# Optimization experiments

Measured on AMD Instinct MI355X. Metric: run time of the kernel, lower is better.

Reference implementation:

```python
import jax, jax.numpy as jnp
import numpy as np

N_NODES = 50000
N_EDGES = 800000
NDIM_IN = 128
EDIM_IN = 128
NDIM_OUT = 128
EDIM_OUT = 128


def setup_inputs() -> dict:
    key = jax.random.key(0)
    ks = jax.random.split(key, 8)
    nfeats = jax.random.normal(ks[0], (N_NODES, NDIM_IN), dtype=jnp.float32)
    efeats = jax.random.normal(ks[1], (N_EDGES, EDIM_IN), dtype=jnp.float32)
    u = jax.random.randint(ks[2], (N_EDGES,), 0, N_NODES, dtype=jnp.int32)
    v = jax.random.randint(ks[3], (N_EDGES,), 0, N_NODES, dtype=jnp.int32)
    # torch.nn.Linear params: weight [out, in], bias [out]
    d_apply_in = 2 * NDIM_IN + EDIM_IN  # concat(nfeats, h_neigh)
    lim1 = 1.0 / np.sqrt(d_apply_in)
    W_apply_w = jax.random.uniform(ks[4], (NDIM_OUT, d_apply_in), jnp.float32, -lim1, lim1)
    W_apply_b = jax.random.uniform(ks[5], (NDIM_OUT,), jnp.float32, -lim1, lim1)
    lim2 = 1.0 / np.sqrt(2 * NDIM_OUT)
    W_edge_w = jax.random.uniform(ks[6], (EDIM_OUT, 2 * NDIM_OUT), jnp.float32, -lim2, lim2)
    W_edge_b = jax.random.uniform(ks[7], (EDIM_OUT,), jnp.float32, -lim2, lim2)
    return {"nfeats": nfeats, "efeats": efeats, "u": u, "v": v,
            "W_apply_w": W_apply_w, "W_apply_b": W_apply_b,
            "W_edge_w": W_edge_w, "W_edge_b": W_edge_b}


def reference(nfeats, efeats, u, v, W_apply_w, W_apply_b, W_edge_w, W_edge_b):
    n_nodes = nfeats.shape[0]
    # message per edge: concat(src node h, edge h)  -> [E, ndim_in+edim_in]
    msg = jnp.concatenate([nfeats[u], efeats], axis=1)
    # mean reduction over incoming edges at dst node v (0 for isolated nodes, like DGL)
    sums = jax.ops.segment_sum(msg, v, num_segments=n_nodes)
    counts = jax.ops.segment_sum(jnp.ones((msg.shape[0],), msg.dtype), v, num_segments=n_nodes)
    h_neigh = jnp.where(counts[:, None] > 0, sums / jnp.maximum(counts, 1.0)[:, None], 0.0)
    # node update
    h_nodes_new = jnp.concatenate([nfeats, h_neigh], axis=1) @ W_apply_w.T + W_apply_b
    h_nodes_new = jax.nn.relu(h_nodes_new)
    # edge update
    edge_input = jnp.concatenate([h_nodes_new[u], h_nodes_new[v]], axis=1)
    h_edges_new = jax.nn.relu(edge_input @ W_edge_w.T + W_edge_b)
    return h_nodes_new, h_edges_new
```

## Files before the change

kernel.cpp:

```cpp
#include <hip/hip_runtime.h>
#include <hip/hip_bf16.h>

#define N_NODES_C 50000
#define N_EDGES_C 800000
#define NBLK_NODES 196
#define EDGE_HEAD_ROWS 50048

typedef __attribute__((ext_vector_type(8))) short bf16x8;
typedef __attribute__((ext_vector_type(4))) float f32x4;

__device__ __forceinline__ unsigned short f2bf(float f) {
    unsigned int x = __float_as_uint(f);
    unsigned int r = x + 0x7fffu + ((x >> 16) & 1u);
    return (unsigned short)(r >> 16);
}
__device__ __forceinline__ float bf2f(unsigned short s) {
    return __uint_as_float(((unsigned int)s) << 16);
}

__global__ __launch_bounds__(256) void setup_k(
    const float* __restrict__ Wa, const float* __restrict__ We,
    unsigned short* __restrict__ wa, unsigned short* __restrict__ we,
    int* __restrict__ cnt)
{
    int b = blockIdx.x, t = threadIdx.x;
    if (b < 196) {
        int i = b * 256 + t;
        if (i < N_NODES_C) cnt[i] = 0;
    } else if (b < 388) {
        int i = (b - 196) * 256 + t;
        wa[i] = f2bf(Wa[i]);
    } else {
        int i = (b - 388) * 256 + t;
        we[i] = f2bf(We[i]);
    }
}

__global__ __launch_bounds__(256) void count_k(const int* __restrict__ v, int* __restrict__ cnt)
{
    int e = blockIdx.x * 256 + threadIdx.x;
    atomicAdd(&cnt[v[e]], 1);
}

__global__ __launch_bounds__(256) void scan_partial_k(
    const int* __restrict__ cnt, int* __restrict__ bsum)
{
    __shared__ int ws[4];
    int b = blockIdx.x, t = threadIdx.x, lane = t & 63, wid = t >> 6;
    int i = b * 256 + t;
    int x = (i < N_NODES_C) ? cnt[i] : 0;
    int s = x;
#pragma unroll
    for (int d = 1; d < 64; d <<= 1) {
        int tv = __shfl_up(s, d, 64);
        if (lane >= d) s += tv;
    }
    if (lane == 63) ws[wid] = s;
    __syncthreads();
    if (t == 0) bsum[b] = ws[0] + ws[1] + ws[2] + ws[3];
}

__global__ __launch_bounds__(256) void scan_block_k(
    const int* __restrict__ bsum, int* __restrict__ boff, int* __restrict__ rowst)
{
    __shared__ int ws[4];
    int t = threadIdx.x, lane = t & 63, wid = t >> 6;
    int x = (t < NBLK_NODES) ? bsum[t] : 0;
    int s = x;
#pragma unroll
    for (int d = 1; d < 64; d <<= 1) {
        int tv = __shfl_up(s, d, 64);
        if (lane >= d) s += tv;
    }
    if (lane == 63) ws[wid] = s;
    __syncthreads();
    if (t == 0) {
        int a = 0;
#pragma unroll
        for (int w = 0; w < 4; ++w) { int tmp = ws[w]; ws[w] = a; a += tmp; }
    }
    __syncthreads();
    int excl = ws[wid] + s - x;
    if (t < NBLK_NODES) boff[t] = excl;
    if (t == 255) rowst[N_NODES_C] = excl;
}

__global__ __launch_bounds__(256) void scan_scatter_k(
    const int* __restrict__ cnt, const int* __restrict__ boff,
    int* __restrict__ rowst, int* __restrict__ cursor)
{
    __shared__ int ws[4];
    int b = blockIdx.x, t = threadIdx.x, lane = t & 63, wid = t >> 6;
    int i = b * 256 + t;
    int x = (i < N_NODES_C) ? cnt[i] : 0;
    int s = x;
#pragma unroll
    for (int d = 1; d < 64; d <<= 1) {
        int tv = __shfl_up(s, d, 64);
        if (lane >= d) s += tv;
    }
    if (lane == 63) ws[wid] = s;
    __syncthreads();
    if (t == 0) {
        int a = 0;
#pragma unroll
        for (int w = 0; w < 4; ++w) { int tmp = ws[w]; ws[w] = a; a += tmp; }
    }
    __syncthreads();
    int excl = boff[b] + ws[wid] + s - x;
    if (i < N_NODES_C) { rowst[i] = excl; cursor[i] = excl; }
}

__global__ __launch_bounds__(256) void fill_k(const int* __restrict__ v,
                                              const int* __restrict__ u,
                                              int* __restrict__ cursor,
                                              int2* __restrict__ pairs)
{
    int e = blockIdx.x * 256 + threadIdx.x;
    int pos = atomicAdd(&cursor[v[e]], 1);
    pairs[pos] = make_int2(e, u[e]);
}

__global__ __launch_bounds__(256) void aggregate_k(
    const int2* __restrict__ pairs, const int* __restrict__ rowst,
    const float* __restrict__ nfeats, const float* __restrict__ efeats,
    unsigned short* __restrict__ hnb)
{
    int wv   = blockIdx.x * 4 + (threadIdx.x >> 6);
    int lane = threadIdx.x & 63;
    if (wv >= N_NODES_C) return;
    int s = rowst[wv], e_end = rowst[wv + 1];
    int deg = e_end - s;

    if (deg == 0) {
        *reinterpret_cast<ushort4*>(hnb + (size_t)wv * 256 + lane * 4) =
            make_ushort4(0, 0, 0, 0);
        return;
    }

    float4 a0 = make_float4(0.f, 0.f, 0.f, 0.f);
    float4 a1 = a0, a2 = a0, a3 = a0;
    for (int base = s; base < e_end; base += 8) {
        int2 p[8];
#pragma unroll
        for (int t = 0; t < 8; ++t) {
            int idx = base + t;
            p[t] = pairs[idx < e_end ? idx : e_end - 1];
        }
        float4 val[8];
#pragma unroll
        for (int t = 0; t < 8; ++t) {
            const float* src = (lane < 32)
                ? (nfeats + (size_t)p[t].y * 128 + lane * 4)
                : (efeats + (size_t)p[t].x * 128 + (lane - 32) * 4);
            val[t] = *reinterpret_cast<const float4*>(src);
        }
#pragma unroll
        for (int t = 0; t < 8; ++t) {
            if (base + t < e_end) {
                float4* a = (t & 2) ? ((t & 1) ? &a3 : &a2)
                                    : ((t & 1) ? &a1 : &a0);
                a->x += val[t].x; a->y += val[t].y;
                a->z += val[t].z; a->w += val[t].w;
            }
        }
    }
    a0.x += a1.x + a2.x + a3.x;
    a0.y += a1.y + a2.y + a3.y;
    a0.z += a1.z + a2.z + a3.z;
    a0.w += a1.w + a2.w + a3.w;
    float r = 1.f / (float)deg;
    ushort4 o;
    o.x = f2bf(a0.x * r); o.y = f2bf(a0.y * r);
    o.z = f2bf(a0.z * r); o.w = f2bf(a0.w * r);
    *reinterpret_cast<ushort4*>(hnb + (size_t)wv * 256 + lane * 4) = o;
}

__device__ __forceinline__ void stage_half_row(
    const float* __restrict__ src, char* __restrict__ lds, int row, int halfg)
{
#pragma unroll
    for (int g = 0; g < 4; ++g) {
        float4 f0 = reinterpret_cast<const float4*>(src)[g * 2 + 0];
        float4 f1 = reinterpret_cast<const float4*>(src)[g * 2 + 1];
        union { unsigned short s[8]; uint4 q; } pk;
        pk.s[0] = f2bf(f0.x); pk.s[1] = f2bf(f0.y);
        pk.s[2] = f2bf(f0.z); pk.s[3] = f2bf(f0.w);
        pk.s[4] = f2bf(f1.x); pk.s[5] = f2bf(f1.y);
        pk.s[6] = f2bf(f1.z); pk.s[7] = f2bf(f1.w);
        int byteoff = ((halfg * 4 + g) * 16) ^ ((row & 7) << 4);
        *reinterpret_cast<uint4*>(lds + row * 128 + byteoff) = pk.q;
    }
}

__device__ __forceinline__ void stage_half_row_cp(
    const unsigned short* __restrict__ src, char* __restrict__ lds, int row, int halfg)
{
#pragma unroll
    for (int g = 0; g < 4; ++g) {
        uint4 q = reinterpret_cast<const uint4*>(src)[g];
        int byteoff = ((halfg * 4 + g) * 16) ^ ((row & 7) << 4);
        *reinterpret_cast<uint4*>(lds + row * 128 + byteoff) = q;
    }
}

__device__ __forceinline__ void mfma_slab(
    const char* __restrict__ Xs, const char* __restrict__ Ws,
    int wm, int wn, int lane, f32x4 (&acc)[4][4])
{
#pragma unroll
    for (int c = 0; c < 2; ++c) {
        int kb = c * 64 + (lane >> 4) * 16;
        bf16x8 a[4], b[4];
#pragma unroll
        for (int i = 0; i < 4; ++i) {
            int row = wm * 64 + i * 16 + (lane & 15);
            a[i] = *reinterpret_cast<const bf16x8*>(
                Xs + row * 128 + (kb ^ ((row & 7) << 4)));
        }
#pragma unroll
        for (int j = 0; j < 4; ++j) {
            int row = wn * 64 + j * 16 + (lane & 15);
            b[j] = *reinterpret_cast<const bf16x8*>(
                Ws + row * 128 + (kb ^ ((row & 7) << 4)));
        }
#pragma unroll
        for (int i = 0; i < 4; ++i)
#pragma unroll
            for (int j = 0; j < 4; ++j)
                acc[i][j] = __builtin_amdgcn_mfma_f32_16x16x32_bf16(
                    a[i], b[j], acc[i][j], 0, 0, 0);
    }
}

__device__ __forceinline__ void epilogue_store(
    const f32x4 (&acc)[4][4], const float* __restrict__ bias,
    float* __restrict__ out, int row_base, int row_limit, int wm, int wn, int lane)
{
    int col0 = wn * 64 + (lane & 15);
    int row0 = row_base + wm * 64 + (lane >> 4) * 4;
#pragma unroll
    for (int j = 0; j < 4; ++j) {
        float bj = bias[col0 + j * 16];
#pragma unroll
        for (int i = 0; i < 4; ++i) {
#pragma unroll
            for (int r = 0; r < 4; ++r) {
                int row = row0 + i * 16 + r;
                if (row < row_limit) {
                    float val = fmaxf(acc[i][j][r] + bj, 0.f);
                    out[(size_t)row * 128 + col0 + j * 16] = val;
                }
            }
        }
    }
}

__global__ __launch_bounds__(256) void node_k(
    const float* __restrict__ nfeats, const unsigned short* __restrict__ hnb,
    const unsigned short* __restrict__ wa, const unsigned short* __restrict__ we,
    const float* __restrict__ bias, float* __restrict__ out,
    unsigned short* __restrict__ P)
{
    __shared__ uint4 XsBuf[1024];
    __shared__ uint4 WsBuf[1024];
    char* Xs = (char*)XsBuf;
    char* Ws = (char*)WsBuf;

    int tid = threadIdx.x;
    int n0  = blockIdx.x * 128;
    int wave = tid >> 6, lane = tid & 63;
    int wm = wave >> 1, wn = wave & 1;
    int srow = tid >> 1, shalf = tid & 1;

    int nrow = n0 + srow;
    if (nrow >= N_NODES_C) nrow = N_NODES_C - 1;

    f32x4 acc[4][4];
#pragma unroll
    for (int i = 0; i < 4; ++i)
#pragma unroll
        for (int j = 0; j < 4; ++j) acc[i][j] = (f32x4)0.f;

#pragma unroll
    for (int k0 = 0; k0 < 384; k0 += 64) {
        if (k0 < 128)
            stage_half_row(nfeats + (size_t)nrow * 128 + k0 + shalf * 32,
                           Xs, srow, shalf);
        else
            stage_half_row_cp(hnb + (size_t)nrow * 256 + (k0 - 128) + shalf * 32,
                              Xs, srow, shalf);
        stage_half_row_cp(wa + (size_t)srow * 384 + k0 + shalf * 32,
                          Ws, srow, shalf);
        __syncthreads();
        mfma_slab(Xs, Ws, wm, wn, lane, acc);
        __syncthreads();
    }

    epilogue_store(acc, bias, out, n0, N_NODES_C, wm, wn, lane);
    __syncthreads();

    int col0 = wn * 64 + (lane & 15);
    int row0 = n0 + wm * 64 + (lane >> 4) * 4;
#pragma unroll
    for (int cb = 0; cb < 2; ++cb) {
        f32x4 accP[4][4];
#pragma unroll
        for (int i = 0; i < 4; ++i)
#pragma unroll
            for (int j = 0; j < 4; ++j) accP[i][j] = (f32x4)0.f;

#pragma unroll
        for (int s2 = 0; s2 < 2; ++s2) {
            int k0 = s2 * 64;
            stage_half_row(out + (size_t)nrow * 128 + k0 + shalf * 32,
                           Xs, srow, shalf);
            stage_half_row_cp(we + (size_t)srow * 256 + cb * 128 + k0 + shalf * 32,
                              Ws, srow, shalf);
            __syncthreads();
            mfma_slab(Xs, Ws, wm, wn, lane, accP);
            __syncthreads();
        }

#pragma unroll
        for (int j = 0; j < 4; ++j) {
#pragma unroll
            for (int i = 0; i < 4; ++i) {
#pragma unroll
                for (int r = 0; r < 4; ++r) {
                    int row = row0 + i * 16 + r;
                    if (row < N_NODES_C)
                        P[(size_t)row * 256 + cb * 128 + col0 + j * 16] =
                            f2bf(accP[i][j][r]);
                }
            }
        }
    }
}

__global__ __launch_bounds__(256) void edge_add_k(
    const unsigned short* __restrict__ P, const int* __restrict__ u,
    const int* __restrict__ v, const float* __restrict__ bias,
    float* __restrict__ out, int e_base)
{
    int c = blockIdx.x * 256 + threadIdx.x;
    int e = e_base + (c >> 5);
    int q = c & 31;
    int uu = u[e], vv = v[e];
    ushort4 pa = *reinterpret_cast<const ushort4*>(P + (size_t)uu * 256 + q * 4);
    ushort4 pb = *reinterpret_cast<const ushort4*>(P + (size_t)vv * 256 + 128 + q * 4);
    float4 b4 = *reinterpret_cast<const float4*>(bias + q * 4);
    float4 o;
    o.x = fmaxf(bf2f(pa.x) + bf2f(pb.x) + b4.x, 0.f);
    o.y = fmaxf(bf2f(pa.y) + bf2f(pb.y) + b4.y, 0.f);
    o.z = fmaxf(bf2f(pa.z) + bf2f(pb.z) + b4.z, 0.f);
    o.w = fmaxf(bf2f(pa.w) + bf2f(pb.w) + b4.w, 0.f);
    *reinterpret_cast<float4*>(out + (size_t)e * 128 + q * 4) = o;
}

__global__ __launch_bounds__(256) void edge_head_k(
    const float* __restrict__ h, const int* __restrict__ u,
    const int* __restrict__ v, const float* __restrict__ W,
    const float* __restrict__ bias, float* __restrict__ out)
{
    __shared__ uint4 XsBuf[1024];
    __shared__ uint4 WsBuf[1024];
    __shared__ int us[128], vs[128];
    char* Xs = (char*)XsBuf;
    char* Ws = (char*)WsBuf;

    int tid = threadIdx.x;
    int e0  = blockIdx.x * 128;
    if (tid < 128) us[tid]       = u[e0 + tid];
    else           vs[tid - 128] = v[e0 + tid - 128];
    __syncthreads();

    int wave = tid >> 6, lane = tid & 63;
    int wm = wave >> 1, wn = wave & 1;
    int srow = tid >> 1, shalf = tid & 1;

    f32x4 acc[4][4];
#pragma unroll
    for (int i = 0; i < 4; ++i)
#pragma unroll
        for (int j = 0; j < 4; ++j) acc[i][j] = (f32x4)0.f;

#pragma unroll
    for (int k0 = 0; k0 < 256; k0 += 64) {
        int node = (k0 < 128) ? us[srow] : vs[srow];
        stage_half_row(h + (size_t)node * 128 + (k0 & 127) + shalf * 32,
                       Xs, srow, shalf);
        stage_half_row(W + (size_t)srow * 256 + k0 + shalf * 32,
                       Ws, srow, shalf);
        __syncthreads();
        mfma_slab(Xs, Ws, wm, wn, lane, acc);
        __syncthreads();
    }

    epilogue_store(acc, bias, out, e0, N_EDGES_C, wm, wn, lane);
}

extern "C" void kernel_launch(void* const* d_in, const int* in_sizes, int n_in,
                              void* d_out, int out_size, void* d_ws, size_t ws_size,
                              hipStream_t stream)
{
    const float* nfeats    = (const float*)d_in[0];
    const float* efeats    = (const float*)d_in[1];
    const int*   u         = (const int*)d_in[2];
    const int*   v         = (const int*)d_in[3];
    const float* W_apply_w = (const float*)d_in[4];
    const float* W_apply_b = (const float*)d_in[5];
    const float* W_edge_w  = (const float*)d_in[6];
    const float* W_edge_b  = (const float*)d_in[7];

    float* out      = (float*)d_out;
    float* h_nodes  = out;
    float* edge_out = out + (size_t)N_NODES_C * 128;

    unsigned short* hnb = (unsigned short*)edge_out;
    int*   cnt     = (int*)(edge_out + 6400000);
    int*   rowst   = cnt + N_NODES_C;
    int*   cursor  = rowst + N_NODES_C + 1;
    int2*  pairs   = (int2*)(cursor + N_NODES_C + 2);
    int*   bsum    = (int*)(pairs + N_EDGES_C);
    int*   boff    = bsum + 256;
    unsigned short* wa = (unsigned short*)(boff + 256);
    unsigned short* we = wa + 49152;

    const size_t P_ELEMS = (size_t)N_NODES_C * 256;
    bool p_in_ws = ws_size >= P_ELEMS * sizeof(unsigned short);
    unsigned short* P = p_in_ws ? (unsigned short*)d_ws
                                : (unsigned short*)edge_out;

    setup_k<<<516, 256, 0, stream>>>(W_apply_w, W_edge_w, wa, we, cnt);
    count_k<<<N_EDGES_C / 256, 256, 0, stream>>>(v, cnt);
    scan_partial_k<<<NBLK_NODES, 256, 0, stream>>>(cnt, bsum);
    scan_block_k<<<1, 256, 0, stream>>>(bsum, boff, rowst);
    scan_scatter_k<<<NBLK_NODES, 256, 0, stream>>>(cnt, boff, rowst, cursor);
    fill_k<<<N_EDGES_C / 256, 256, 0, stream>>>(v, u, cursor, pairs);
    aggregate_k<<<N_NODES_C / 4, 256, 0, stream>>>(pairs, rowst, nfeats, efeats, hnb);

    node_k<<<(N_NODES_C + 127) / 128, 256, 0, stream>>>(
        nfeats, hnb, wa, we, W_apply_b, h_nodes, P);

    if (p_in_ws) {
        edge_add_k<<<N_EDGES_C * 32 / 256, 256, 0, stream>>>(
            P, u, v, W_edge_b, edge_out, 0);
    } else {
        edge_add_k<<<(N_EDGES_C - EDGE_HEAD_ROWS) * 32 / 256, 256, 0, stream>>>(
            P, u, v, W_edge_b, edge_out, EDGE_HEAD_ROWS);
        edge_head_k<<<EDGE_HEAD_ROWS / 128, 256, 0, stream>>>(
            h_nodes, u, v, W_edge_w, W_edge_b, edge_out);
    }
}
```

Measured before the change: 409.2 us.

## Walk edges in destination-sorted CSR order for the final edge add

Replaces the per-edge gather kernel with a CSR-driven kernel where each wave handles one destination node. The destination half of the projected features plus bias is loaded once per node and reused across all incoming edges, and four source rows are fetched per iteration to keep more loads in flight. Output rows are written scattered by edge id instead of contiguously, and pairs/rowst move into the workspace, so the workspace requirement grows and the fallback head split changes.

```diff
diff --git a/kernel.cpp b/kernel.cpp
--- a/kernel.cpp
+++ b/kernel.cpp
@@ -4,7 +4,7 @@
 #define N_NODES_C 50000
 #define N_EDGES_C 800000
 #define NBLK_NODES 196
-#define EDGE_HEAD_ROWS 50048
+#define EDGE_HEAD_ROWS 64128
 
 typedef __attribute__((ext_vector_type(8))) short bf16x8;
 typedef __attribute__((ext_vector_type(4))) float f32x4;
@@ -338,24 +338,51 @@
     }
 }
 
-__global__ __launch_bounds__(256) void edge_add_k(
-    const unsigned short* __restrict__ P, const int* __restrict__ u,
-    const int* __restrict__ v, const float* __restrict__ bias,
-    float* __restrict__ out, int e_base)
-{
-    int c = blockIdx.x * 256 + threadIdx.x;
-    int e = e_base + (c >> 5);
-    int q = c & 31;
-    int uu = u[e], vv = v[e];
-    ushort4 pa = *reinterpret_cast<const ushort4*>(P + (size_t)uu * 256 + q * 4);
-    ushort4 pb = *reinterpret_cast<const ushort4*>(P + (size_t)vv * 256 + 128 + q * 4);
-    float4 b4 = *reinterpret_cast<const float4*>(bias + q * 4);
-    float4 o;
-    o.x = fmaxf(bf2f(pa.x) + bf2f(pb.x) + b4.x, 0.f);
-    o.y = fmaxf(bf2f(pa.y) + bf2f(pb.y) + b4.y, 0.f);
-    o.z = fmaxf(bf2f(pa.z) + bf2f(pb.z) + b4.z, 0.f);
-    o.w = fmaxf(bf2f(pa.w) + bf2f(pb.w) + b4.w, 0.f);
-    *reinterpret_cast<float4*>(out + (size_t)e * 128 + q * 4) = o;
+__global__ __launch_bounds__(256) void edge_csr_k(
+    const int2* __restrict__ pairs, const int* __restrict__ rowst,
+    const unsigned short* __restrict__ P, const float* __restrict__ bias,
+    float* __restrict__ out, int e_min)
+{
+    int wv   = blockIdx.x * 4 + (threadIdx.x >> 6);
+    int lane = threadIdx.x & 63;
+    int l32  = lane & 31, half = lane >> 5;
+    if (wv >= N_NODES_C) return;
+    int s = rowst[wv], e_end = rowst[wv + 1];
+    if (s + half >= e_end) return;
+
+    ushort4 q2 = *reinterpret_cast<const ushort4*>(P + (size_t)wv * 256 + 128 + l32 * 4);
+    float4  b4 = *reinterpret_cast<const float4*>(bias + l32 * 4);
+    float t2x = bf2f(q2.x) + b4.x;
+    float t2y = bf2f(q2.y) + b4.y;
+    float t2z = bf2f(q2.z) + b4.z;
+    float t2w = bf2f(q2.w) + b4.w;
+
+    for (int base = s + half; base < e_end; base += 8) {
+        int2 pr[4];
+#pragma unroll
+        for (int t = 0; t < 4; ++t) {
+            int idx = base + t * 2;
+            pr[t] = pairs[idx < e_end ? idx : e_end - 1];
+        }
+        ushort4 p1[4];
+#pragma unroll
+        for (int t = 0; t < 4; ++t)
+            p1[t] = *reinterpret_cast<const ushort4*>(
+                P + (size_t)pr[t].y * 256 + l32 * 4);
+#pragma unroll
+        for (int t = 0; t < 4; ++t) {
+            int idx = base + t * 2;
+            if (idx < e_end && pr[t].x >= e_min) {
+                float4 o;
+                o.x = fmaxf(bf2f(p1[t].x) + t2x, 0.f);
+                o.y = fmaxf(bf2f(p1[t].y) + t2y, 0.f);
+                o.z = fmaxf(bf2f(p1[t].z) + t2z, 0.f);
+                o.w = fmaxf(bf2f(p1[t].w) + t2w, 0.f);
+                *reinterpret_cast<float4*>(
+                    out + (size_t)pr[t].x * 128 + l32 * 4) = o;
+            }
+        }
+    }
 }
 
 __global__ __launch_bounds__(256) void edge_head_k(
@@ -419,18 +446,23 @@
 
     unsigned short* hnb = (unsigned short*)edge_out;
     int*   cnt     = (int*)(edge_out + 6400000);
-    int*   rowst   = cnt + N_NODES_C;
-    int*   cursor  = rowst + N_NODES_C + 1;
-    int2*  pairs   = (int2*)(cursor + N_NODES_C + 2);
-    int*   bsum    = (int*)(pairs + N_EDGES_C);
+    int*   cursor  = cnt + N_NODES_C;
+    int*   bsum    = cursor + N_NODES_C;
     int*   boff    = bsum + 256;
     unsigned short* wa = (unsigned short*)(boff + 256);
     unsigned short* we = wa + 49152;
-
-    const size_t P_ELEMS = (size_t)N_NODES_C * 256;
-    bool p_in_ws = ws_size >= P_ELEMS * sizeof(unsigned short);
-    unsigned short* P = p_in_ws ? (unsigned short*)d_ws
-                                : (unsigned short*)edge_out;
+    unsigned short* P_fb     = (unsigned short*)edge_out;
+    int2*           pairs_fb = (int2*)(we + 32768);
+    int*            rowst_fb = (int*)(pairs_fb + N_EDGES_C);
+
+    const size_t WS_NEED = (size_t)N_NODES_C * 256 * 2
+                         + (size_t)N_EDGES_C * 8
+                         + (size_t)(N_NODES_C + 1) * 4;
+    bool use_ws = ws_size >= WS_NEED;
+    unsigned short* P     = use_ws ? (unsigned short*)d_ws : P_fb;
+    int2*           pairs = use_ws ? (int2*)((char*)d_ws + (size_t)N_NODES_C * 512)
+                                   : pairs_fb;
+    int*            rowst = use_ws ? (int*)(pairs + N_EDGES_C) : rowst_fb;
 
     setup_k<<<516, 256, 0, stream>>>(W_apply_w, W_edge_w, wa, we, cnt);
     count_k<<<N_EDGES_C / 256, 256, 0, stream>>>(v, cnt);
@@ -443,12 +475,12 @@
     node_k<<<(N_NODES_C + 127) / 128, 256, 0, stream>>>(
         nfeats, hnb, wa, we, W_apply_b, h_nodes, P);
 
-    if (p_in_ws) {
-        edge_add_k<<<N_EDGES_C * 32 / 256, 256, 0, stream>>>(
-            P, u, v, W_edge_b, edge_out, 0);
+    if (use_ws) {
+        edge_csr_k<<<N_NODES_C / 4, 256, 0, stream>>>(
+            pairs, rowst, P, W_edge_b, edge_out, 0);
     } else {
-        edge_add_k<<<(N_EDGES_C - EDGE_HEAD_ROWS) * 32 / 256, 256, 0, stream>>>(
-            P, u, v, W_edge_b, edge_out, EDGE_HEAD_ROWS);
+        edge_csr_k<<<N_NODES_C / 4, 256, 0, stream>>>(
+            pairs, rowst, P, W_edge_b, edge_out, EDGE_HEAD_ROWS);
         edge_head_k<<<EDGE_HEAD_ROWS / 128, 256, 0, stream>>>(
             h_nodes, u, v, W_edge_w, W_edge_b, edge_out);
     }
```

Result: faster. 398.2 us (-2.7%).
